# Optimization experiments

Hardware: AMD Instinct MI355X
Metric: run time of the kernel (lower is better)

## Reference

```python
import jax, jax.numpy as jnp
import numpy as np

HIDDEN = 128
D = 3


def _safe_norm(diff):
    # norm over last axis with NaN-free value at diff==0 (diagonal, masked out later)
    s = jnp.sum(diff * diff, axis=-1, keepdims=True)
    return jnp.sqrt(jnp.where(s > 0, s, 1.0)) * (s > 0)


def setup_inputs() -> dict:
    key = jax.random.key(0)
    ks = jax.random.split(key, 7)
    B, N = 4, 512
    pos_scaled = jax.random.normal(ks[0], (B, N, D), dtype=jnp.float32)
    # edge-MLP params: Linear(2,H) -> SiLU -> Linear(H,H) -> SiLU -> Linear(H,1)
    W1 = jax.random.normal(ks[1], (2, HIDDEN), dtype=jnp.float32) / np.sqrt(2.0)
    b1 = jnp.zeros((HIDDEN,), dtype=jnp.float32)
    W2 = jax.random.normal(ks[2], (HIDDEN, HIDDEN), dtype=jnp.float32) / np.sqrt(HIDDEN)
    b2 = jnp.zeros((HIDDEN,), dtype=jnp.float32)
    W3 = jax.random.normal(ks[3], (HIDDEN, 1), dtype=jnp.float32) / np.sqrt(HIDDEN)
    b3 = jnp.zeros((1,), dtype=jnp.float32)
    return {"pos_scaled": pos_scaled, "W1": W1, "b1": b1, "W2": W2, "b2": b2,
            "W3": W3, "b3": b3}


def reference(pos_scaled, W1, b1, W2, b2, W3, b3):
    B, N, _ = pos_scaled.shape
    diff = pos_scaled[:, :, None, :] - pos_scaled[:, None, :, :]   # [B,N,N,D]
    dist = _safe_norm(diff)                                        # [B,N,N,1]
    dist_safe = jnp.clip(dist, 1e-4, 50.0)
    feat = jnp.concatenate([dist_safe, 1.0 / dist_safe], axis=-1)  # [B,N,N,2]
    h = jax.nn.silu(feat @ W1 + b1)                                # [B,N,N,H]
    h = jax.nn.silu(h @ W2 + b2)                                   # [B,N,N,H]
    mag = h @ W3 + b3                                              # [B,N,N,1]
    mask = (~jnp.eye(N, dtype=bool))[None, :, :, None]
    pair_forces = mag * (diff / jnp.clip(dist, 1e-6, None)) * mask # [B,N,N,D]
    return jnp.sum(pair_forces, axis=2)                            # [B,N,D]
```

## Files before the change

### kernel.cpp

```cpp
#include <hip/hip_runtime.h>

#define H       128
#define NPTS    512
#define NBATCH  4
#define BLOCK   256
#define WAVES   4
#define PW      8

#define TSAMP   8192
#define TIVL    8191
#define T0      (-13.2877123795f)
#define TRANGE  (18.9315685693f)
#define TABLE_FLOATS (2 * TSAMP)
#define TABLE_BYTES  (TABLE_FLOATS * 4u)

__device__ __forceinline__ float fast_rcp(float x) { return __builtin_amdgcn_rcpf(x); }

__device__ __forceinline__ float silu_f(float x) {
    float e = __expf(-x);
    return x * fast_rcp(1.0f + e);
}

__global__ __launch_bounds__(BLOCK) void build_mag_table(
    const float* __restrict__ W1, const float* __restrict__ b1,
    const float* __restrict__ W2, const float* __restrict__ b2,
    const float* __restrict__ W3, const float* __restrict__ b3,
    float* __restrict__ tab)
{
    __shared__ float W2s[H * H];
    __shared__ float W1s[2 * H];
    __shared__ float b1s[H], b2s[H], W3s[H];
    __shared__ float h1s[WAVES][H][PW];

    const int tid  = threadIdx.x;
    const int lane = tid & 63;
    const int w    = tid >> 6;

    {
        const float4* src = (const float4*)W2;
        float4* dst = (float4*)W2s;
        #pragma unroll
        for (int r = 0; r < (H * H / 4) / BLOCK; ++r)
            dst[r * BLOCK + tid] = src[r * BLOCK + tid];
        if (tid < 2 * H) W1s[tid] = W1[tid];
        if (tid < H) { b1s[tid] = b1[tid]; b2s[tid] = b2[tid]; W3s[tid] = W3[tid]; }
    }

    const float b3v = b3[0];
    const int base  = blockIdx.x * (WAVES * PW) + w * PW;

    __syncthreads();

    float d8[PW], in8[PW];
    #pragma unroll
    for (int p = 0; p < PW; ++p) {
        float t  = fmaf((float)(base + p), TRANGE / (float)TIVL, T0);
        float d  = exp2f(t);
        float ds = fminf(fmaxf(d, 1e-4f), 50.0f);
        d8[p]  = ds;
        in8[p] = 1.0f / ds;
    }

    #pragma unroll
    for (int kk = 0; kk < 2; ++kk) {
        const int ch = lane + kk * 64;
        const float wa = W1s[ch], wb = W1s[H + ch], bb = b1s[ch];
        float v[PW];
        #pragma unroll
        for (int p = 0; p < PW; ++p)
            v[p] = silu_f(fmaf(d8[p], wa, fmaf(in8[p], wb, bb)));
        float4* dst = (float4*)&h1s[w][ch][0];
        dst[0] = make_float4(v[0], v[1], v[2], v[3]);
        dst[1] = make_float4(v[4], v[5], v[6], v[7]);
    }

    const int k0 = 2 * lane;
    float acc0[PW], acc1[PW];
    #pragma unroll
    for (int p = 0; p < PW; ++p) { acc0[p] = 0.f; acc1[p] = 0.f; }

    #pragma unroll 4
    for (int j = 0; j < H; ++j) {
        const float4 ha = *(const float4*)&h1s[w][j][0];
        const float4 hb = *(const float4*)&h1s[w][j][4];
        const float2 ww = *(const float2*)&W2s[j * H + k0];
        const float wx = ww.x, wy = ww.y;
        acc0[0] = fmaf(ha.x, wx, acc0[0]); acc1[0] = fmaf(ha.x, wy, acc1[0]);
        acc0[1] = fmaf(ha.y, wx, acc0[1]); acc1[1] = fmaf(ha.y, wy, acc1[1]);
        acc0[2] = fmaf(ha.z, wx, acc0[2]); acc1[2] = fmaf(ha.z, wy, acc1[2]);
        acc0[3] = fmaf(ha.w, wx, acc0[3]); acc1[3] = fmaf(ha.w, wy, acc1[3]);
        acc0[4] = fmaf(hb.x, wx, acc0[4]); acc1[4] = fmaf(hb.x, wy, acc1[4]);
        acc0[5] = fmaf(hb.y, wx, acc0[5]); acc1[5] = fmaf(hb.y, wy, acc1[5]);
        acc0[6] = fmaf(hb.z, wx, acc0[6]); acc1[6] = fmaf(hb.z, wy, acc1[6]);
        acc0[7] = fmaf(hb.w, wx, acc0[7]); acc1[7] = fmaf(hb.w, wy, acc1[7]);
    }

    const float b20 = b2s[k0], b21 = b2s[k0 + 1];
    const float w30 = W3s[k0], w31 = W3s[k0 + 1];
    float part[PW];
    #pragma unroll
    for (int p = 0; p < PW; ++p)
        part[p] = silu_f(acc0[p] + b20) * w30 + silu_f(acc1[p] + b21) * w31;

    #pragma unroll
    for (int off = 32; off >= 1; off >>= 1) {
        #pragma unroll
        for (int p = 0; p < PW; ++p)
            part[p] += __shfl_xor(part[p], off);
    }

    if (lane == 0) {
        #pragma unroll
        for (int p = 0; p < PW; ++p) {
            const int k = base + p;
            const float g = part[p] + b3v;
            if (k < TIVL) tab[2 * k] = g;
            if (k >= 1)   tab[2 * k - 1] = g;
        }
    }
}

__global__ __launch_bounds__(BLOCK) void eval_forces(
    const float* __restrict__ pos, const float* __restrict__ tab,
    float* __restrict__ out)
{
    __shared__ float poss[NPTS * 3];

    const int tid  = threadIdx.x;
    const int lane = tid & 63;
    const int w    = tid >> 6;
    const int row  = blockIdx.x * WAVES + w;
    const int b    = row >> 9;
    const int i    = row & (NPTS - 1);

    {
        const float4* src = (const float4*)(pos + b * NPTS * 3);
        float4* dst = (float4*)poss;
        for (int r = tid; r < NPTS * 3 / 4; r += BLOCK) dst[r] = src[r];
    }
    __syncthreads();

    const float pix = poss[3 * i + 0];
    const float piy = poss[3 * i + 1];
    const float piz = poss[3 * i + 2];

    const float INVH = (float)TIVL / TRANGE;
    const float XOFF = -T0 * ((float)TIVL / TRANGE);
    const float2* tab2 = (const float2*)tab;

    float fx = 0.f, fy = 0.f, fz = 0.f;

    #pragma unroll
    for (int k = 0; k < NPTS / 64; ++k) {
        const int j = lane + 64 * k;
        const float dx = pix - poss[3 * j + 0];
        const float dy = piy - poss[3 * j + 1];
        const float dz = piz - poss[3 * j + 2];
        const float s  = fmaf(dx, dx, fmaf(dy, dy, dz * dz));
        const bool ok  = (s > 0.0f) && (j != i);
        const float rs = __builtin_amdgcn_rsqf(fmaxf(s, 1e-30f));
        const float d  = s * rs;
        const float ds = fminf(fmaxf(d, 1e-4f), 50.0f);
        float x = fmaf(__log2f(ds), INVH, XOFF);
        x = fminf(fmaxf(x, 0.0f), (float)TIVL - 0.001f);
        const int   kk = (int)x;
        const float fr = x - (float)kk;
        const float2 g = tab2[kk];
        const float mag = fmaf(fr, g.y - g.x, g.x);
        const float f   = ok ? mag * fminf(rs, 1e6f) : 0.0f;
        fx = fmaf(f, dx, fx);
        fy = fmaf(f, dy, fy);
        fz = fmaf(f, dz, fz);
    }

    #pragma unroll
    for (int off = 32; off >= 1; off >>= 1) {
        fx += __shfl_xor(fx, off);
        fy += __shfl_xor(fy, off);
        fz += __shfl_xor(fz, off);
    }
    if (lane == 0) {
        out[row * 3 + 0] = fx;
        out[row * 3 + 1] = fy;
        out[row * 3 + 2] = fz;
    }
}

extern "C" void kernel_launch(void* const* d_in, const int* in_sizes, int n_in,
                              void* d_out, int out_size, void* d_ws, size_t ws_size,
                              hipStream_t stream) {
    const float* pos = (const float*)d_in[0];
    const float* W1  = (const float*)d_in[1];
    const float* b1  = (const float*)d_in[2];
    const float* W2  = (const float*)d_in[3];
    const float* b2  = (const float*)d_in[4];
    const float* W3  = (const float*)d_in[5];
    const float* b3  = (const float*)d_in[6];
    float* out = (float*)d_out;
    float* tab = (float*)d_ws;

    hipLaunchKernelGGL(build_mag_table, dim3(TSAMP / (WAVES * PW)), dim3(BLOCK), 0, stream,
                       W1, b1, W2, b2, W3, b3, tab);
    hipLaunchKernelGGL(eval_forces, dim3(NBATCH * NPTS / WAVES), dim3(BLOCK), 0, stream,
                       pos, tab, out);
}
```

Measured before the change: 76.26 us.

## Drop LDS staging in table build; broadcast hidden activations via readlane

The table-building kernel no longer copies the 64KB W2 matrix and the other weights into shared memory, and no longer needs a block barrier. Each wave reads W2 rows directly from global memory (L2-cached, coalesced float2 per lane). The first-layer activations stay in registers and are broadcast with readlane instead of being staged through LDS. This removes the 64KB LDS footprint, which limited occupancy, along with the per-block copy cost. In exchange it adds repeated global loads of W2 per wave and scalar readlane instructions in the inner loop.

```diff
diff --git a/kernel.cpp b/kernel.cpp
--- a/kernel.cpp
+++ b/kernel.cpp
@@ -11,8 +11,6 @@
 #define TIVL    8191
 #define T0      (-13.2877123795f)
 #define TRANGE  (18.9315685693f)
-#define TABLE_FLOATS (2 * TSAMP)
-#define TABLE_BYTES  (TABLE_FLOATS * 4u)
 
 __device__ __forceinline__ float fast_rcp(float x) { return __builtin_amdgcn_rcpf(x); }
 
@@ -21,35 +19,20 @@
     return x * fast_rcp(1.0f + e);
 }
 
+__device__ __forceinline__ float bcast_lane(float v, int src) {
+    return __uint_as_float(__builtin_amdgcn_readlane(__float_as_uint(v), src));
+}
+
 __global__ __launch_bounds__(BLOCK) void build_mag_table(
     const float* __restrict__ W1, const float* __restrict__ b1,
     const float* __restrict__ W2, const float* __restrict__ b2,
     const float* __restrict__ W3, const float* __restrict__ b3,
     float* __restrict__ tab)
 {
-    __shared__ float W2s[H * H];
-    __shared__ float W1s[2 * H];
-    __shared__ float b1s[H], b2s[H], W3s[H];
-    __shared__ float h1s[WAVES][H][PW];
-
     const int tid  = threadIdx.x;
     const int lane = tid & 63;
     const int w    = tid >> 6;
-
-    {
-        const float4* src = (const float4*)W2;
-        float4* dst = (float4*)W2s;
-        #pragma unroll
-        for (int r = 0; r < (H * H / 4) / BLOCK; ++r)
-            dst[r * BLOCK + tid] = src[r * BLOCK + tid];
-        if (tid < 2 * H) W1s[tid] = W1[tid];
-        if (tid < H) { b1s[tid] = b1[tid]; b2s[tid] = b2[tid]; W3s[tid] = W3[tid]; }
-    }
-
-    const float b3v = b3[0];
-    const int base  = blockIdx.x * (WAVES * PW) + w * PW;
-
-    __syncthreads();
+    const int base = blockIdx.x * (WAVES * PW) + w * PW;
 
     float d8[PW], in8[PW];
     #pragma unroll
@@ -61,17 +44,13 @@
         in8[p] = 1.0f / ds;
     }
 
+    const float wa0 = W1[lane],      wb0 = W1[H + lane],      bb0 = b1[lane];
+    const float wa1 = W1[lane + 64], wb1 = W1[H + lane + 64], bb1 = b1[lane + 64];
+    float ha[PW], hb[PW];
     #pragma unroll
-    for (int kk = 0; kk < 2; ++kk) {
-        const int ch = lane + kk * 64;
-        const float wa = W1s[ch], wb = W1s[H + ch], bb = b1s[ch];
-        float v[PW];
-        #pragma unroll
-        for (int p = 0; p < PW; ++p)
-            v[p] = silu_f(fmaf(d8[p], wa, fmaf(in8[p], wb, bb)));
-        float4* dst = (float4*)&h1s[w][ch][0];
-        dst[0] = make_float4(v[0], v[1], v[2], v[3]);
-        dst[1] = make_float4(v[4], v[5], v[6], v[7]);
+    for (int p = 0; p < PW; ++p) {
+        ha[p] = silu_f(fmaf(d8[p], wa0, fmaf(in8[p], wb0, bb0)));
+        hb[p] = silu_f(fmaf(d8[p], wa1, fmaf(in8[p], wb1, bb1)));
     }
 
     const int k0 = 2 * lane;
@@ -79,24 +58,31 @@
     #pragma unroll
     for (int p = 0; p < PW; ++p) { acc0[p] = 0.f; acc1[p] = 0.f; }
 
-    #pragma unroll 4
-    for (int j = 0; j < H; ++j) {
-        const float4 ha = *(const float4*)&h1s[w][j][0];
-        const float4 hb = *(const float4*)&h1s[w][j][4];
-        const float2 ww = *(const float2*)&W2s[j * H + k0];
-        const float wx = ww.x, wy = ww.y;
-        acc0[0] = fmaf(ha.x, wx, acc0[0]); acc1[0] = fmaf(ha.x, wy, acc1[0]);
-        acc0[1] = fmaf(ha.y, wx, acc0[1]); acc1[1] = fmaf(ha.y, wy, acc1[1]);
-        acc0[2] = fmaf(ha.z, wx, acc0[2]); acc1[2] = fmaf(ha.z, wy, acc1[2]);
-        acc0[3] = fmaf(ha.w, wx, acc0[3]); acc1[3] = fmaf(ha.w, wy, acc1[3]);
-        acc0[4] = fmaf(hb.x, wx, acc0[4]); acc1[4] = fmaf(hb.x, wy, acc1[4]);
-        acc0[5] = fmaf(hb.y, wx, acc0[5]); acc1[5] = fmaf(hb.y, wy, acc1[5]);
-        acc0[6] = fmaf(hb.z, wx, acc0[6]); acc1[6] = fmaf(hb.z, wy, acc1[6]);
-        acc0[7] = fmaf(hb.w, wx, acc0[7]); acc1[7] = fmaf(hb.w, wy, acc1[7]);
+    const float2* w2v = (const float2*)W2;
+
+    #pragma unroll 16
+    for (int j = 0; j < 64; ++j) {
+        const float2 ww = w2v[j * 64 + lane];
+        #pragma unroll
+        for (int p = 0; p < PW; ++p) {
+            const float hv = bcast_lane(ha[p], j);
+            acc0[p] = fmaf(hv, ww.x, acc0[p]);
+            acc1[p] = fmaf(hv, ww.y, acc1[p]);
+        }
+    }
+    #pragma unroll 16
+    for (int j = 0; j < 64; ++j) {
+        const float2 ww = w2v[(j + 64) * 64 + lane];
+        #pragma unroll
+        for (int p = 0; p < PW; ++p) {
+            const float hv = bcast_lane(hb[p], j);
+            acc0[p] = fmaf(hv, ww.x, acc0[p]);
+            acc1[p] = fmaf(hv, ww.y, acc1[p]);
+        }
     }
 
-    const float b20 = b2s[k0], b21 = b2s[k0 + 1];
-    const float w30 = W3s[k0], w31 = W3s[k0 + 1];
+    const float b20 = b2[k0], b21 = b2[k0 + 1];
+    const float w30 = W3[k0], w31 = W3[k0 + 1];
     float part[PW];
     #pragma unroll
     for (int p = 0; p < PW; ++p)
@@ -110,6 +96,7 @@
     }
 
     if (lane == 0) {
+        const float b3v = b3[0];
         #pragma unroll
         for (int p = 0; p < PW; ++p) {
             const int k = base + p;
```

New measurement: 78.07 us. 1.02x slower.
